# Performance work log

Measured on AMD Instinct MI355X. Metric: run time of the kernel, lower is better.

The kernel has to match this reference:

```python
import jax, jax.numpy as jnp
import numpy as np
import math

EMBED_DIM = 256
NUM_HEADS = 32
D_K = EMBED_DIM // NUM_HEADS  # 8 qubits per head circuit


def setup_inputs() -> dict:
    key = jax.random.key(0)
    k1, k2, k3, k4 = jax.random.split(key, 4)
    B, S = 2, 2048
    x = jax.random.normal(k1, (B, S, EMBED_DIM), dtype=jnp.float32)
    mask = jnp.ones((B, S), dtype=jnp.int32)
    # trainable RX angles, one per wire, shared across heads (single _QLayer instance)
    theta = jax.random.normal(k2, (D_K,), dtype=jnp.float32)
    # out_proj Linear(embed_dim, embed_dim) with bias
    bound = 1.0 / math.sqrt(EMBED_DIM)
    W_out = jax.random.uniform(k3, (EMBED_DIM, EMBED_DIM), dtype=jnp.float32, minval=-bound, maxval=bound)
    b_out = jax.random.uniform(k4, (EMBED_DIM,), dtype=jnp.float32, minval=-bound, maxval=bound)
    return {"x": x, "mask": mask, "theta": theta, "W_out": W_out, "b_out": b_out}


def reference(x, mask, theta, W_out, b_out):
    B, S, E = x.shape
    H, dk = NUM_HEADS, D_K
    # [B, H, S, d_k]
    xh = x.reshape(B, S, H, dk).transpose(0, 2, 1, 3)
    # Quantum circuit per element: RX(x) then RX(theta) on |0>, measure PauliZ.
    # Product state => <Z_i> = cos(x_i + theta_i). Exact closed form.
    q = jnp.cos(xh + theta)  # [B, H, S, dk]
    scores = jnp.einsum('bhqd,bhkd->bhqk', q, q) / jnp.float32(math.sqrt(dk))
    scores = jnp.where(mask[:, None, None, :] == 0, jnp.float32(-1e9), scores)
    attn = jax.nn.softmax(scores, axis=-1)  # dropout is identity in eval mode
    out = jnp.einsum('bhqk,bhkd->bhqd', attn, q)
    out = out.transpose(0, 2, 1, 3).reshape(B, S, E)
    return out @ W_out.T + b_out
```

## Files before the change

### kernel.cpp

```cpp
#include <hip/hip_runtime.h>

#define B_ 2
#define S_ 2048
#define E_ 256
#define H_ 32
#define DK_ 8

typedef float f32x4 __attribute__((ext_vector_type(4)));
typedef short short8 __attribute__((ext_vector_type(8)));
typedef unsigned short us8 __attribute__((ext_vector_type(8)));

#define SQ_ 0.71419638f
#define CONES_F 0.71484375f
#define CONES_BITS 0x3F373F37u
#define CORR_ (CONES_F / SQ_)

static __device__ __forceinline__ unsigned short f2bf(float x) {
  unsigned u = __float_as_uint(x);
  return (unsigned short)((u + 0x7FFFu + ((u >> 16) & 1u)) >> 16);
}

static __device__ __forceinline__ float ex2(float x) {
#if __has_builtin(__builtin_amdgcn_exp2f)
  return __builtin_amdgcn_exp2f(x);
#else
  float r; asm("v_exp_f32 %0, %1\n\ts_nop 0" : "=v"(r) : "v"(x)); return r;
#endif
}

static __device__ __forceinline__ unsigned cvtpk(float lo, float hi) {
  unsigned r;
  asm("v_cvt_pk_bf16_f32 %0, %1, %2" : "=v"(r) : "v"(lo), "v"(hi));
  return r;
}

__global__ __launch_bounds__(256) void qgen3(
    const float* __restrict__ x, const float* __restrict__ theta,
    unsigned short* __restrict__ qb) {
  __shared__ unsigned short TL[16][264];

  const int tid = threadIdx.x;
  const int gs = blockIdx.x * 16;
  const int b = gs >> 11, s0 = gs & (S_ - 1);

  float th[8];
#pragma unroll
  for (int d = 0; d < 8; ++d) th[d] = theta[d];

#pragma unroll
  for (int p = 0; p < 4; ++p) {
    int fi = tid + p * 256;
    int row = fi >> 6, col4 = fi & 63;
    float4 v = *(const float4*)&x[((size_t)(b * S_ + s0 + row)) * E_ + col4 * 4];
    int dbase = (col4 & 1) * 4;
    unsigned w0 = (unsigned)f2bf(__cosf(v.x + th[dbase + 0]) * SQ_) |
                  ((unsigned)f2bf(__cosf(v.y + th[dbase + 1]) * SQ_) << 16);
    unsigned w1 = (unsigned)f2bf(__cosf(v.z + th[dbase + 2]) * SQ_) |
                  ((unsigned)f2bf(__cosf(v.w + th[dbase + 3]) * SQ_) << 16);
    uint2 wv; wv.x = w0; wv.y = w1;
    *(uint2*)&TL[row][col4 * 4] = wv;
  }
  __syncthreads();

  const int h = tid >> 3, part = tid & 7;
#pragma unroll
  for (int i = 0; i < 2; ++i) {
    int r = part * 2 + i;
    uint4 t = *(uint4*)&TL[r][h * 8];
    *(uint4*)&qb[((size_t)(b * H_ + h) * S_ + s0 + r) * DK_] = t;
  }
}

__global__ __launch_bounds__(256) void attn3(
    const unsigned short* __restrict__ qb, const int* __restrict__ mask,
    float* __restrict__ ao) {
  __shared__ float4 K4[S_];
  __shared__ unsigned short KTs[DK_ * 2056];
  __shared__ float biasS[S_];

  const int bh = blockIdx.x >> 3;
  const int qblk = (blockIdx.x & 7) * 256;
  const int b = bh >> 5, h = bh & 31;
  const int tid = threadIdx.x;

  const float4* qbv = (const float4*)(qb + (size_t)bh * S_ * DK_);
#pragma unroll
  for (int p = 0; p < 4; ++p) {
    int rp = tid + p * 256;
    int s = rp * 2;
    float4 f0 = qbv[s], f1 = qbv[s + 1];
    K4[s] = f0; K4[s + 1] = f1;
    us8 u0 = __builtin_bit_cast(us8, f0);
    us8 u1 = __builtin_bit_cast(us8, f1);
#pragma unroll
    for (int d = 0; d < 8; ++d) {
      unsigned wv = (unsigned)u0[d] | ((unsigned)u1[d] << 16);
      *(unsigned*)&KTs[d * 2056 + s] = wv;
    }
  }
  const int* mb = mask + b * S_;
  for (int i = tid; i < S_; i += 256) biasS[i] = mb[i] ? 0.0f : -1.0e9f;
  __syncthreads();

  const int wid = tid >> 6, lane = tid & 63;
  const int c = lane & 15, g = lane >> 4;

  const float4 zero4 = make_float4(0.f, 0.f, 0.f, 0.f);
  uint4 cpat; cpat.x = CONES_BITS; cpat.y = CONES_BITS;
  cpat.z = CONES_BITS; cpat.w = CONES_BITS;

  const int qrow0 = qblk + wid * 64;
  short8 qf[4];
  f32x4 acc[4];
#pragma unroll
  for (int qt = 0; qt < 4; ++qt) {
    float4 t = zero4;
    if (lane < 16) t = K4[qrow0 + qt * 16 + lane];
    qf[qt] = __builtin_bit_cast(short8, t);
    acc[qt] = (f32x4){0.f, 0.f, 0.f, 0.f};
  }

  const f32x4 zf = {0.f, 0.f, 0.f, 0.f};

  for (int kt = 0; kt < 64; ++kt) {
    float4 a0f = K4[kt * 32 + c];
    float4 a1f = K4[kt * 32 + 16 + c];
    float4 vtf;
    if (c < 8)       vtf = *(const float4*)&KTs[c * 2056 + kt * 32 + 8 * g];
    else if (c == 8) vtf = __builtin_bit_cast(float4, cpat);
    else             vtf = zero4;
    float4 bias0 = *(const float4*)&biasS[kt * 32 + g * 4];
    float4 bias1 = *(const float4*)&biasS[kt * 32 + 16 + g * 4];

    short8 aK0 = __builtin_bit_cast(short8, a0f);
    short8 aK1 = __builtin_bit_cast(short8, a1f);
    short8 aV  = __builtin_bit_cast(short8, vtf);

#pragma unroll
    for (int qt = 0; qt < 4; ++qt) {
      f32x4 s0 = __builtin_amdgcn_mfma_f32_16x16x32_bf16(aK0, qf[qt], zf, 0, 0, 0);
      f32x4 s1 = __builtin_amdgcn_mfma_f32_16x16x32_bf16(aK1, qf[qt], zf, 0, 0, 0);
      unsigned w0 = cvtpk(ex2(s0[0] + bias0.x), ex2(s0[1] + bias0.y));
      unsigned w1 = cvtpk(ex2(s0[2] + bias0.z), ex2(s0[3] + bias0.w));
      unsigned w2 = cvtpk(ex2(s1[0] + bias1.x), ex2(s1[1] + bias1.y));
      unsigned w3 = cvtpk(ex2(s1[2] + bias1.z), ex2(s1[3] + bias1.w));
      asm("v_permlane32_swap_b32 %0, %1" : "+v"(w0), "+v"(w2));
      asm("v_permlane16_swap_b32 %0, %1" : "+v"(w0), "+v"(w2));
      asm("v_permlane32_swap_b32 %0, %1" : "+v"(w1), "+v"(w3));
      asm("v_permlane16_swap_b32 %0, %1" : "+v"(w1), "+v"(w3));
      uint4 pu; pu.x = w0; pu.y = w1; pu.z = w2; pu.w = w3;
      acc[qt] = __builtin_amdgcn_mfma_f32_16x16x32_bf16(
          aV, __builtin_bit_cast(short8, pu), acc[qt], 0, 0, 0);
    }
  }

#pragma unroll
  for (int qt = 0; qt < 4; ++qt) {
    float den = __shfl(acc[qt][0], 32 + c);
    float rd = CORR_ / den;
    if (g < 2) {
      int qrow = qrow0 + qt * 16 + c;
      float4 o;
      o.x = acc[qt][0] * rd; o.y = acc[qt][1] * rd;
      o.z = acc[qt][2] * rd; o.w = acc[qt][3] * rd;
      *(float4*)&ao[((size_t)(b * S_ + qrow)) * E_ + h * DK_ + g * 4] = o;
    }
  }
}

#define BM 64
#define BN 64
#define BKk 64
#define LDP 68

__global__ __launch_bounds__(256) void outproj_kernel(
    const float* __restrict__ A, const float* __restrict__ W,
    const float* __restrict__ bias, float* __restrict__ C) {
  __shared__ float As[BKk][LDP];
  __shared__ float Ws[BKk][LDP];

  const int nbn = E_ / BN;
  const int bm = blockIdx.x / nbn;
  const int bn = blockIdx.x % nbn;
  const int tid = threadIdx.x;
  const int tm = tid >> 4, tn = tid & 15;
  const int m0 = tm * 4, n0 = tn * 4;

  float acc[4][4] = {};

  for (int kt = 0; kt < E_; kt += BKk) {
#pragma unroll
    for (int f = 0; f < 4; ++f) {
      int fi = tid + f * 256;
      int row = fi >> 4;
      int kk = (fi & 15) << 2;
      float4 v = *(const float4*)&A[(size_t)(bm * BM + row) * E_ + kt + kk];
      As[kk + 0][row] = v.x; As[kk + 1][row] = v.y;
      As[kk + 2][row] = v.z; As[kk + 3][row] = v.w;
      float4 wv = *(const float4*)&W[(size_t)(bn * BN + row) * E_ + kt + kk];
      Ws[kk + 0][row] = wv.x; Ws[kk + 1][row] = wv.y;
      Ws[kk + 2][row] = wv.z; Ws[kk + 3][row] = wv.w;
    }
    __syncthreads();

#pragma unroll 8
    for (int kk = 0; kk < BKk; ++kk) {
      float4 a = *(const float4*)&As[kk][m0];
      float4 w = *(const float4*)&Ws[kk][n0];
      float ar[4] = {a.x, a.y, a.z, a.w};
      float wr[4] = {w.x, w.y, w.z, w.w};
#pragma unroll
      for (int i = 0; i < 4; ++i)
#pragma unroll
        for (int j = 0; j < 4; ++j)
          acc[i][j] = fmaf(ar[i], wr[j], acc[i][j]);
    }
    __syncthreads();
  }

  float4 bv = *(const float4*)&bias[bn * BN + n0];
  float br[4] = {bv.x, bv.y, bv.z, bv.w};
#pragma unroll
  for (int i = 0; i < 4; ++i) {
    int m = bm * BM + m0 + i;
    float4 outv = make_float4(acc[i][0] + br[0], acc[i][1] + br[1],
                              acc[i][2] + br[2], acc[i][3] + br[3]);
    *(float4*)&C[(size_t)m * E_ + bn * BN + n0] = outv;
  }
}

extern "C" void kernel_launch(void* const* d_in, const int* in_sizes, int n_in,
                              void* d_out, int out_size, void* d_ws, size_t ws_size,
                              hipStream_t stream) {
  const float* x     = (const float*)d_in[0];
  const int*   mask  = (const int*)d_in[1];
  const float* theta = (const float*)d_in[2];
  const float* W     = (const float*)d_in[3];
  const float* bvec  = (const float*)d_in[4];
  float* out = (float*)d_out;

  unsigned short* qbb = (unsigned short*)d_ws;
  float* ao = (float*)(qbb + (size_t)B_ * H_ * S_ * DK_);

  qgen3<<<256, 256, 0, stream>>>(x, theta, qbb);
  attn3<<<B_ * H_ * 8, 256, 0, stream>>>(qbb, mask, ao);
  outproj_kernel<<<(B_ * S_ / BM) * (E_ / BN), 256, 0, stream>>>(ao, W, bvec, out);
}
```

Baseline: 135.0 us.

## Shrink per-block work across all kernels and add mask-free fast path

All three kernels are resized to launch twice as many blocks: qgen handles 8 rows per block, attention handles 128 queries per block and stages keys in two 1024-row chunks, and outproj uses 32-row tiles. The attention kernel swaps the additive float bias for a bitmask AND on the bf16 probabilities, and it skips masking entirely when a whole chunk is unmasked. qgen uses the hardware packed bf16 convert in place of software rounding. The aim is better occupancy and CU fill on a small problem, at the cost of loading K/V once per block more often and an extra barrier per chunk.

```diff
diff --git a/kernel.cpp b/kernel.cpp
--- a/kernel.cpp
+++ b/kernel.cpp
@@ -14,11 +14,6 @@
 #define CONES_F 0.71484375f
 #define CONES_BITS 0x3F373F37u
 #define CORR_ (CONES_F / SQ_)
-
-static __device__ __forceinline__ unsigned short f2bf(float x) {
-  unsigned u = __float_as_uint(x);
-  return (unsigned short)((u + 0x7FFFu + ((u >> 16) & 1u)) >> 16);
-}
 
 static __device__ __forceinline__ float ex2(float x) {
 #if __has_builtin(__builtin_amdgcn_exp2f)
@@ -34,13 +29,13 @@
   return r;
 }
 
-__global__ __launch_bounds__(256) void qgen3(
+__global__ __launch_bounds__(256) void qgen4(
     const float* __restrict__ x, const float* __restrict__ theta,
     unsigned short* __restrict__ qb) {
-  __shared__ unsigned short TL[16][264];
+  __shared__ unsigned short TL[8][264];
 
   const int tid = threadIdx.x;
-  const int gs = blockIdx.x * 16;
+  const int gs = blockIdx.x * 8;
   const int b = gs >> 11, s0 = gs & (S_ - 1);
 
   float th[8];
@@ -48,60 +43,37 @@
   for (int d = 0; d < 8; ++d) th[d] = theta[d];
 
 #pragma unroll
-  for (int p = 0; p < 4; ++p) {
+  for (int p = 0; p < 2; ++p) {
     int fi = tid + p * 256;
     int row = fi >> 6, col4 = fi & 63;
     float4 v = *(const float4*)&x[((size_t)(b * S_ + s0 + row)) * E_ + col4 * 4];
     int dbase = (col4 & 1) * 4;
-    unsigned w0 = (unsigned)f2bf(__cosf(v.x + th[dbase + 0]) * SQ_) |
-                  ((unsigned)f2bf(__cosf(v.y + th[dbase + 1]) * SQ_) << 16);
-    unsigned w1 = (unsigned)f2bf(__cosf(v.z + th[dbase + 2]) * SQ_) |
-                  ((unsigned)f2bf(__cosf(v.w + th[dbase + 3]) * SQ_) << 16);
-    uint2 wv; wv.x = w0; wv.y = w1;
+    uint2 wv;
+    wv.x = cvtpk(__cosf(v.x + th[dbase + 0]) * SQ_,
+                 __cosf(v.y + th[dbase + 1]) * SQ_);
+    wv.y = cvtpk(__cosf(v.z + th[dbase + 2]) * SQ_,
+                 __cosf(v.w + th[dbase + 3]) * SQ_);
     *(uint2*)&TL[row][col4 * 4] = wv;
   }
   __syncthreads();
 
-  const int h = tid >> 3, part = tid & 7;
-#pragma unroll
-  for (int i = 0; i < 2; ++i) {
-    int r = part * 2 + i;
-    uint4 t = *(uint4*)&TL[r][h * 8];
-    *(uint4*)&qb[((size_t)(b * H_ + h) * S_ + s0 + r) * DK_] = t;
-  }
-}
-
-__global__ __launch_bounds__(256) void attn3(
+  const int h = tid >> 3, r = tid & 7;
+  uint4 t = *(uint4*)&TL[r][h * 8];
+  *(uint4*)&qb[((size_t)(b * H_ + h) * S_ + s0 + r) * DK_] = t;
+}
+
+__global__ __launch_bounds__(256) void attn4(
     const unsigned short* __restrict__ qb, const int* __restrict__ mask,
     float* __restrict__ ao) {
-  __shared__ float4 K4[S_];
-  __shared__ unsigned short KTs[DK_ * 2056];
-  __shared__ float biasS[S_];
-
-  const int bh = blockIdx.x >> 3;
-  const int qblk = (blockIdx.x & 7) * 256;
+  __shared__ float4 K4[1024];
+  __shared__ unsigned short KTs[DK_ * 1040];
+  __shared__ unsigned Mk[512];
+  __shared__ int sOK[4];
+
+  const int bh = blockIdx.x >> 4;
+  const int qblk = (blockIdx.x & 15) * 128;
   const int b = bh >> 5, h = bh & 31;
   const int tid = threadIdx.x;
-
-  const float4* qbv = (const float4*)(qb + (size_t)bh * S_ * DK_);
-#pragma unroll
-  for (int p = 0; p < 4; ++p) {
-    int rp = tid + p * 256;
-    int s = rp * 2;
-    float4 f0 = qbv[s], f1 = qbv[s + 1];
-    K4[s] = f0; K4[s + 1] = f1;
-    us8 u0 = __builtin_bit_cast(us8, f0);
-    us8 u1 = __builtin_bit_cast(us8, f1);
-#pragma unroll
-    for (int d = 0; d < 8; ++d) {
-      unsigned wv = (unsigned)u0[d] | ((unsigned)u1[d] << 16);
-      *(unsigned*)&KTs[d * 2056 + s] = wv;
-    }
-  }
-  const int* mb = mask + b * S_;
-  for (int i = tid; i < S_; i += 256) biasS[i] = mb[i] ? 0.0f : -1.0e9f;
-  __syncthreads();
-
   const int wid = tid >> 6, lane = tid & 63;
   const int c = lane & 15, g = lane >> 4;
 
@@ -109,53 +81,90 @@
   uint4 cpat; cpat.x = CONES_BITS; cpat.y = CONES_BITS;
   cpat.z = CONES_BITS; cpat.w = CONES_BITS;
 
-  const int qrow0 = qblk + wid * 64;
-  short8 qf[4];
-  f32x4 acc[4];
-#pragma unroll
-  for (int qt = 0; qt < 4; ++qt) {
+  const float4* qbv = (const float4*)(qb + (size_t)bh * S_ * DK_);
+
+  const int qrow0 = qblk + wid * 32;
+  short8 qf[2];
+  f32x4 acc[2];
+#pragma unroll
+  for (int qt = 0; qt < 2; ++qt) {
     float4 t = zero4;
-    if (lane < 16) t = K4[qrow0 + qt * 16 + lane];
+    if (lane < 16) t = qbv[qrow0 + qt * 16 + lane];
     qf[qt] = __builtin_bit_cast(short8, t);
     acc[qt] = (f32x4){0.f, 0.f, 0.f, 0.f};
   }
 
   const f32x4 zf = {0.f, 0.f, 0.f, 0.f};
 
-  for (int kt = 0; kt < 64; ++kt) {
-    float4 a0f = K4[kt * 32 + c];
-    float4 a1f = K4[kt * 32 + 16 + c];
-    float4 vtf;
-    if (c < 8)       vtf = *(const float4*)&KTs[c * 2056 + kt * 32 + 8 * g];
-    else if (c == 8) vtf = __builtin_bit_cast(float4, cpat);
-    else             vtf = zero4;
-    float4 bias0 = *(const float4*)&biasS[kt * 32 + g * 4];
-    float4 bias1 = *(const float4*)&biasS[kt * 32 + 16 + g * 4];
-
-    short8 aK0 = __builtin_bit_cast(short8, a0f);
-    short8 aK1 = __builtin_bit_cast(short8, a1f);
-    short8 aV  = __builtin_bit_cast(short8, vtf);
-
-#pragma unroll
-    for (int qt = 0; qt < 4; ++qt) {
-      f32x4 s0 = __builtin_amdgcn_mfma_f32_16x16x32_bf16(aK0, qf[qt], zf, 0, 0, 0);
-      f32x4 s1 = __builtin_amdgcn_mfma_f32_16x16x32_bf16(aK1, qf[qt], zf, 0, 0, 0);
-      unsigned w0 = cvtpk(ex2(s0[0] + bias0.x), ex2(s0[1] + bias0.y));
-      unsigned w1 = cvtpk(ex2(s0[2] + bias0.z), ex2(s0[3] + bias0.w));
-      unsigned w2 = cvtpk(ex2(s1[0] + bias1.x), ex2(s1[1] + bias1.y));
-      unsigned w3 = cvtpk(ex2(s1[2] + bias1.z), ex2(s1[3] + bias1.w));
-      asm("v_permlane32_swap_b32 %0, %1" : "+v"(w0), "+v"(w2));
-      asm("v_permlane16_swap_b32 %0, %1" : "+v"(w0), "+v"(w2));
-      asm("v_permlane32_swap_b32 %0, %1" : "+v"(w1), "+v"(w3));
-      asm("v_permlane16_swap_b32 %0, %1" : "+v"(w1), "+v"(w3));
-      uint4 pu; pu.x = w0; pu.y = w1; pu.z = w2; pu.w = w3;
-      acc[qt] = __builtin_amdgcn_mfma_f32_16x16x32_bf16(
-          aV, __builtin_bit_cast(short8, pu), acc[qt], 0, 0, 0);
-    }
-  }
-
-#pragma unroll
-  for (int qt = 0; qt < 4; ++qt) {
+#define KLOOP(MASKED)                                                        \
+  for (int kt = 0; kt < 32; ++kt) {                                          \
+    float4 a0f = K4[kt * 32 + c];                                            \
+    float4 a1f = K4[kt * 32 + 16 + c];                                       \
+    float4 vtf;                                                              \
+    if (c < 8)       vtf = *(const float4*)&KTs[c * 1040 + kt * 32 + 8 * g]; \
+    else if (c == 8) vtf = __builtin_bit_cast(float4, cpat);                 \
+    else             vtf = zero4;                                            \
+    uint2 mA, mB;                                                            \
+    if (MASKED) {                                                            \
+      mA = *(const uint2*)&Mk[kt * 16 + 2 * g];                              \
+      mB = *(const uint2*)&Mk[kt * 16 + 8 + 2 * g];                          \
+    }                                                                        \
+    short8 aK0 = __builtin_bit_cast(short8, a0f);                            \
+    short8 aK1 = __builtin_bit_cast(short8, a1f);                            \
+    short8 aV  = __builtin_bit_cast(short8, vtf);                            \
+    _Pragma("unroll")                                                        \
+    for (int qt = 0; qt < 2; ++qt) {                                         \
+      f32x4 s0 = __builtin_amdgcn_mfma_f32_16x16x32_bf16(aK0, qf[qt], zf, 0, 0, 0); \
+      f32x4 s1 = __builtin_amdgcn_mfma_f32_16x16x32_bf16(aK1, qf[qt], zf, 0, 0, 0); \
+      unsigned w0 = cvtpk(ex2(s0[0]), ex2(s0[1]));                           \
+      unsigned w1 = cvtpk(ex2(s0[2]), ex2(s0[3]));                           \
+      unsigned w2 = cvtpk(ex2(s1[0]), ex2(s1[1]));                           \
+      unsigned w3 = cvtpk(ex2(s1[2]), ex2(s1[3]));                           \
+      if (MASKED) { w0 &= mA.x; w1 &= mA.y; w2 &= mB.x; w3 &= mB.y; }        \
+      asm("v_permlane32_swap_b32 %0, %1" : "+v"(w0), "+v"(w2));              \
+      asm("v_permlane16_swap_b32 %0, %1" : "+v"(w0), "+v"(w2));              \
+      asm("v_permlane32_swap_b32 %0, %1" : "+v"(w1), "+v"(w3));              \
+      asm("v_permlane16_swap_b32 %0, %1" : "+v"(w1), "+v"(w3));              \
+      uint4 pu; pu.x = w0; pu.y = w1; pu.z = w2; pu.w = w3;                  \
+      acc[qt] = __builtin_amdgcn_mfma_f32_16x16x32_bf16(                     \
+          aV, __builtin_bit_cast(short8, pu), acc[qt], 0, 0, 0);             \
+    }                                                                        \
+  }
+
+#pragma unroll 1
+  for (int p = 0; p < 2; ++p) {
+    if (p) __syncthreads();
+    const float4* src = qbv + p * 1024;
+#pragma unroll
+    for (int it = 0; it < 2; ++it) {
+      int rp = tid + it * 256;
+      int s = rp * 2;
+      float4 f0 = src[s], f1 = src[s + 1];
+      K4[s] = f0; K4[s + 1] = f1;
+      us8 u0 = __builtin_bit_cast(us8, f0);
+      us8 u1 = __builtin_bit_cast(us8, f1);
+#pragma unroll
+      for (int d = 0; d < 8; ++d) {
+        unsigned wv = (unsigned)u0[d] | ((unsigned)u1[d] << 16);
+        *(unsigned*)&KTs[d * 1040 + s] = wv;
+      }
+    }
+    const int* mp = mask + b * S_ + p * 1024;
+    int4 mv = *(const int4*)&mp[tid * 4];
+    int ok = (mv.x != 0) & (mv.y != 0) & (mv.z != 0) & (mv.w != 0);
+    Mk[2 * tid]     = (mv.x ? 0xFFFFu : 0u) | (mv.y ? 0xFFFF0000u : 0u);
+    Mk[2 * tid + 1] = (mv.z ? 0xFFFFu : 0u) | (mv.w ? 0xFFFF0000u : 0u);
+    int wall = __all(ok);
+    if (lane == 0) sOK[wid] = wall;
+    __syncthreads();
+    int allones = sOK[0] & sOK[1] & sOK[2] & sOK[3];
+
+    if (allones) { KLOOP(0) } else { KLOOP(1) }
+  }
+#undef KLOOP
+
+#pragma unroll
+  for (int qt = 0; qt < 2; ++qt) {
     float den = __shfl(acc[qt][0], 32 + c);
     float rd = CORR_ / den;
     if (g < 2) {
@@ -168,49 +177,49 @@
   }
 }
 
-#define BM 64
-#define BN 64
-#define BKk 64
-#define LDP 68
-
-__global__ __launch_bounds__(256) void outproj_kernel(
+__global__ __launch_bounds__(256) void outproj2(
     const float* __restrict__ A, const float* __restrict__ W,
     const float* __restrict__ bias, float* __restrict__ C) {
-  __shared__ float As[BKk][LDP];
-  __shared__ float Ws[BKk][LDP];
-
-  const int nbn = E_ / BN;
-  const int bm = blockIdx.x / nbn;
-  const int bn = blockIdx.x % nbn;
+  __shared__ float As[64][36];
+  __shared__ float Ws[64][68];
+
+  const int bm = blockIdx.x >> 2;
+  const int bn = blockIdx.x & 3;
   const int tid = threadIdx.x;
   const int tm = tid >> 4, tn = tid & 15;
-  const int m0 = tm * 4, n0 = tn * 4;
-
-  float acc[4][4] = {};
-
-  for (int kt = 0; kt < E_; kt += BKk) {
+  const int m0 = tm * 2, n0 = tn * 4;
+
+  float acc[2][4] = {};
+
+  for (int kt = 0; kt < E_; kt += 64) {
+#pragma unroll
+    for (int f = 0; f < 2; ++f) {
+      int fi = tid + f * 256;
+      int row = fi >> 4;
+      int kk = (fi & 15) << 2;
+      float4 v = *(const float4*)&A[(size_t)(bm * 32 + row) * E_ + kt + kk];
+      As[kk + 0][row] = v.x; As[kk + 1][row] = v.y;
+      As[kk + 2][row] = v.z; As[kk + 3][row] = v.w;
+    }
 #pragma unroll
     for (int f = 0; f < 4; ++f) {
       int fi = tid + f * 256;
       int row = fi >> 4;
       int kk = (fi & 15) << 2;
-      float4 v = *(const float4*)&A[(size_t)(bm * BM + row) * E_ + kt + kk];
-      As[kk + 0][row] = v.x; As[kk + 1][row] = v.y;
-      As[kk + 2][row] = v.z; As[kk + 3][row] = v.w;
-      float4 wv = *(const float4*)&W[(size_t)(bn * BN + row) * E_ + kt + kk];
+      float4 wv = *(const float4*)&W[(size_t)(bn * 64 + row) * E_ + kt + kk];
       Ws[kk + 0][row] = wv.x; Ws[kk + 1][row] = wv.y;
       Ws[kk + 2][row] = wv.z; Ws[kk + 3][row] = wv.w;
     }
     __syncthreads();
 
 #pragma unroll 8
-    for (int kk = 0; kk < BKk; ++kk) {
-      float4 a = *(const float4*)&As[kk][m0];
+    for (int kk = 0; kk < 64; ++kk) {
+      float2 a = *(const float2*)&As[kk][m0];
       float4 w = *(const float4*)&Ws[kk][n0];
-      float ar[4] = {a.x, a.y, a.z, a.w};
+      float ar[2] = {a.x, a.y};
       float wr[4] = {w.x, w.y, w.z, w.w};
 #pragma unroll
-      for (int i = 0; i < 4; ++i)
+      for (int i = 0; i < 2; ++i)
 #pragma unroll
         for (int j = 0; j < 4; ++j)
           acc[i][j] = fmaf(ar[i], wr[j], acc[i][j]);
@@ -218,14 +227,14 @@
     __syncthreads();
   }
 
-  float4 bv = *(const float4*)&bias[bn * BN + n0];
+  float4 bv = *(const float4*)&bias[bn * 64 + n0];
   float br[4] = {bv.x, bv.y, bv.z, bv.w};
 #pragma unroll
-  for (int i = 0; i < 4; ++i) {
-    int m = bm * BM + m0 + i;
+  for (int i = 0; i < 2; ++i) {
+    int m = bm * 32 + m0 + i;
     float4 outv = make_float4(acc[i][0] + br[0], acc[i][1] + br[1],
                               acc[i][2] + br[2], acc[i][3] + br[3]);
-    *(float4*)&C[(size_t)m * E_ + bn * BN + n0] = outv;
+    *(float4*)&C[(size_t)m * E_ + bn * 64 + n0] = outv;
   }
 }
 
@@ -242,7 +251,7 @@
   unsigned short* qbb = (unsigned short*)d_ws;
   float* ao = (float*)(qbb + (size_t)B_ * H_ * S_ * DK_);
 
-  qgen3<<<256, 256, 0, stream>>>(x, theta, qbb);
-  attn3<<<B_ * H_ * 8, 256, 0, stream>>>(qbb, mask, ao);
-  outproj_kernel<<<(B_ * S_ / BM) * (E_ / BN), 256, 0, stream>>>(ao, W, bvec, out);
-}
+  qgen4<<<512, 256, 0, stream>>>(x, theta, qbb);
+  attn4<<<1024, 256, 0, stream>>>(qbb, mask, ao);
+  outproj2<<<512, 256, 0, stream>>>(ao, W, bvec, out);
+}
```

Measured after the change: 130.2 us. 1.04x faster.
